# Optimization experiments

Hardware: AMD Instinct MI355X
Metric: run time of the kernel (lower is better)

Reference implementation:

```python
import jax, jax.numpy as jnp
import numpy as np

N = 50000   # total residue nodes across the batch of peptides
E = 800000  # total directed intra-peptide edges (avg degree 16)
D = 512


def _w(k, shape):
    fan_in = shape[0]
    return (jax.random.normal(k, shape, jnp.float32) / np.sqrt(fan_in)).astype(jnp.float32)


def setup_inputs() -> dict:
    key = jax.random.key(0)
    ks = jax.random.split(key, 12)
    return {
        "peptide_feature": jax.random.normal(ks[0], (N, D), jnp.float32),
        "edge_index": jax.random.randint(ks[1], (2, E), 0, N),
        # aanet_proj: 512 -> 1024 -> 1024 -> 512 -> 80 (ReLU between, none after last)
        "W1": _w(ks[2], (512, 1024)), "b1": jnp.zeros((1024,), jnp.float32),
        "W2": _w(ks[3], (1024, 1024)), "b2": jnp.zeros((1024,), jnp.float32),
        "W3": _w(ks[4], (1024, 512)), "b3": jnp.zeros((512,), jnp.float32),
        "W4": _w(ks[5], (512, 80)), "b4": jnp.zeros((80,), jnp.float32),
        # in_net: 80 -> 512
        "Win": _w(ks[6], (80, 512)), "bin_": jnp.zeros((512,), jnp.float32),
        # GIN conv MLP: 512 -> 512 -> 512 (eps = 0)
        "Wg1": _w(ks[7], (512, 512)), "bg1": jnp.zeros((512,), jnp.float32),
        "Wg2": _w(ks[8], (512, 512)), "bg2": jnp.zeros((512,), jnp.float32),
        # out_net: 512 -> 80
        "Wout": _w(ks[9], (512, 80)), "bout": jnp.zeros((80,), jnp.float32),
    }


def reference(peptide_feature, edge_index, W1, b1, W2, b2, W3, b3, W4, b4,
              Win, bin_, Wg1, bg1, Wg2, bg2, Wout, bout):
    relu = jax.nn.relu
    # aanet_proj
    h = relu(peptide_feature @ W1 + b1)
    h = relu(h @ W2 + b2)
    h = relu(h @ W3 + b3)
    peptide_feat = h @ W4 + b4                      # [N, 80]
    # in_net
    x = peptide_feat @ Win + bin_                   # [N, 512]
    # GIN message passing (sum aggregation, eps=0): per-sample loop in the
    # original is equivalent to one global pass since edges are sample-local.
    src, dst = edge_index[0], edge_index[1]
    agg = jax.ops.segment_sum(x[src], dst, num_segments=N)   # [N, 512]
    g = x + agg
    g = relu(g @ Wg1 + bg1) @ Wg2 + bg2             # GIN MLP
    # out_net
    peptide_mask = g @ Wout + bout                  # [N, 80]
    return peptide_mask, peptide_feat
```

## Files before the change

### kernel.cpp

```cpp
#include <hip/hip_runtime.h>
#include <stdint.h>


using bf16x8 = __attribute__((ext_vector_type(8))) short;
using f32x4  = __attribute__((ext_vector_type(4))) float;

__device__ inline unsigned short f2bf(float f) {
    union { float f; unsigned u; } v; v.f = f;
    unsigned u = v.u;
    u += 0x7FFFu + ((u >> 16) & 1u);
    return (unsigned short)(u >> 16);
}
__device__ inline float bf2f(unsigned u16) {
    return __uint_as_float(u16 << 16);
}

struct PreDescs {
    const float* W[8]; unsigned short* Wt[8];
    int K[8], M[8], Kp[8], ntx[8], start[8];
    int tEnd, cEnd, eEnd;
    const float* feat; unsigned short* featb; int nFeat;
    const int* ei; int E; int* cnt;
};

__global__ __launch_bounds__(256) void rg_preprocess(PreDescs d) {
    int b = blockIdx.x;
    int tid = threadIdx.x;
    if (b < d.tEnd) {
        __shared__ float t[32][33];
        int di = 0;
#pragma unroll
        for (int i = 1; i < 8; ++i) if (b >= d.start[i]) di = i;
        int local = b - d.start[di];
        int bx = local % d.ntx[di];
        int by = local / d.ntx[di];
        const float* W = d.W[di];
        unsigned short* Wt = d.Wt[di];
        int K = d.K[di], M = d.M[di], Kp = d.Kp[di];
        int mb = bx * 32, kb = by * 32;
        int tx = tid & 31, tg = tid >> 5;
#pragma unroll
        for (int p = 0; p < 4; ++p) {
            int r = tg + p * 8;
            int k = kb + r, m = mb + tx;
            t[r][tx] = (k < K && m < M) ? W[(size_t)k * M + m] : 0.f;
        }
        __syncthreads();
#pragma unroll
        for (int p = 0; p < 4; ++p) {
            int r = tg + p * 8;
            int mo = mb + r, ko = kb + tx;
            Wt[(size_t)mo * Kp + ko] = f2bf(t[tx][r]);
        }
    } else if (b < d.cEnd) {
        int i = ((b - d.tEnd) * 256 + tid) * 4;
        if (i + 3 < d.nFeat) {
            float4 v = *(const float4*)(d.feat + i);
            ushort4 o; o.x = f2bf(v.x); o.y = f2bf(v.y); o.z = f2bf(v.z); o.w = f2bf(v.w);
            *(ushort4*)(d.featb + i) = o;
        }
    } else {
        int e = (b - d.cEnd) * 256 + tid;
        if (e < d.E) atomicAdd(&d.cnt[d.ei[d.E + e]], 1);
    }
}

template <bool RELU, bool OUT_BF, bool OUT_F32, bool DEGB, int MT>
__device__ __forceinline__ void gemm_body(
    int bid,
    const unsigned short* __restrict__ A, const unsigned short* __restrict__ Bt,
    const float* __restrict__ bias, const int* __restrict__ deg, int Mvalid,
    unsigned short* __restrict__ outB, float* __restrict__ outF,
    int Nrows, int Kp, int Mp, int gN)
{
    __shared__ __align__(16) unsigned short As[128 * 64];
    __shared__ __align__(16) unsigned short Bs[128 * 64];

    int xcd = bid & 7;
    int slot = bid >> 3;
    int c = slot % MT;
    int rsub = slot / MT;
    int rt = rsub * 8 + xcd;
    if (rt >= gN) return;
    const int rowBase = rt * 128;
    const int nBase   = c * 128;

    const int tid  = threadIdx.x;
    const int lane = tid & 63;
    const int w    = tid >> 6;
    const int wm   = w & 1, wn = w >> 1;

    f32x4 acc[4][4];
#pragma unroll
    for (int i = 0; i < 4; ++i)
#pragma unroll
        for (int j = 0; j < 4; ++j) acc[i][j] = (f32x4){0.f, 0.f, 0.f, 0.f};

    const int nkt = Kp >> 6;
    for (int kt = 0; kt < nkt; ++kt) {
        __syncthreads();
        const int k0 = kt * 64;
#pragma unroll
        for (int i = 0; i < 4; ++i) {
            int q   = i * 256 + tid;
            int r   = q >> 3;
            int cbg = (q & 7) ^ (r & 7);
            const unsigned short* gp = A + (size_t)(rowBase + r) * Kp + k0 + cbg * 8;
            __builtin_amdgcn_global_load_lds(
                (const __attribute__((address_space(1))) void*)gp,
                (__attribute__((address_space(3))) void*)(&As[q * 8]), 16, 0, 0);
        }
#pragma unroll
        for (int i = 0; i < 4; ++i) {
            int q   = i * 256 + tid;
            int r   = q >> 3;
            int cbg = (q & 7) ^ (r & 7);
            const unsigned short* gp = Bt + (size_t)(nBase + r) * Kp + k0 + cbg * 8;
            __builtin_amdgcn_global_load_lds(
                (const __attribute__((address_space(1))) void*)gp,
                (__attribute__((address_space(3))) void*)(&Bs[q * 8]), 16, 0, 0);
        }
        __syncthreads();
#pragma unroll
        for (int kk = 0; kk < 2; ++kk) {
            bf16x8 a[4], b[4];
            const int cb = kk * 4 + (lane >> 4);
#pragma unroll
            for (int i = 0; i < 4; ++i) {
                int r = wm * 64 + i * 16 + (lane & 15);
                a[i] = *(const bf16x8*)&As[(r * 8 + (cb ^ (r & 7))) * 8];
            }
#pragma unroll
            for (int j = 0; j < 4; ++j) {
                int r = wn * 64 + j * 16 + (lane & 15);
                b[j] = *(const bf16x8*)&Bs[(r * 8 + (cb ^ (r & 7))) * 8];
            }
#pragma unroll
            for (int i = 0; i < 4; ++i)
#pragma unroll
                for (int j = 0; j < 4; ++j)
                    acc[i][j] = __builtin_amdgcn_mfma_f32_16x16x32_bf16(b[j], a[i], acc[i][j], 0, 0, 0);
        }
    }

    const int quad = lane >> 4;
#pragma unroll
    for (int i = 0; i < 4; ++i) {
        int row = rowBase + wm * 64 + i * 16 + (lane & 15);
        if (row >= Nrows) continue;
        float sc = 1.f;
        if (DEGB) sc = 1.f + (float)deg[row];
#pragma unroll
        for (int j = 0; j < 4; ++j) {
            int colb = nBase + wn * 64 + j * 16 + quad * 4;
            float4 bv = (colb < Mvalid) ? *(const float4*)(bias + colb)
                                        : (float4){0.f, 0.f, 0.f, 0.f};
            float v0 = acc[i][j][0] + sc * bv.x;
            float v1 = acc[i][j][1] + sc * bv.y;
            float v2 = acc[i][j][2] + sc * bv.z;
            float v3 = acc[i][j][3] + sc * bv.w;
            if (RELU) {
                v0 = v0 > 0.f ? v0 : 0.f; v1 = v1 > 0.f ? v1 : 0.f;
                v2 = v2 > 0.f ? v2 : 0.f; v3 = v3 > 0.f ? v3 : 0.f;
            }
            if (OUT_BF) {
                ushort4 o; o.x = f2bf(v0); o.y = f2bf(v1); o.z = f2bf(v2); o.w = f2bf(v3);
                *(ushort4*)(outB + (size_t)row * Mp + colb) = o;
            }
            if (OUT_F32) {
                if (colb < Mvalid)
                    *(float4*)(outF + (size_t)row * Mvalid + colb) = (float4){v0, v1, v2, v3};
            }
        }
    }
}

template <bool RELU, bool OUT_BF, bool OUT_F32, bool DEGB, int MT>
__global__ __launch_bounds__(256) void rg_gemm(
    const unsigned short* __restrict__ A, const unsigned short* __restrict__ Bt,
    const float* __restrict__ bias, const int* __restrict__ deg, int Mvalid,
    unsigned short* __restrict__ outB, float* __restrict__ outF,
    int Nrows, int Kp, int Mp, int gN)
{
    gemm_body<RELU, OUT_BF, OUT_F32, DEGB, MT>(blockIdx.x, A, Bt, bias, deg,
                                               Mvalid, outB, outF, Nrows, Kp, Mp, gN);
}

__global__ __launch_bounds__(256) void rg_gemm_l1_scatter(
    const unsigned short* __restrict__ A, const unsigned short* __restrict__ Bt,
    const float* __restrict__ bias, int Mvalid,
    unsigned short* __restrict__ outB, int Nrows, int Kp, int Mp, int gN,
    int gemmBlocks, const int* __restrict__ ei, int E,
    int* __restrict__ cursor, int* __restrict__ cols)
{
    int bid = blockIdx.x;
    if (bid < gemmBlocks) {
        gemm_body<true, true, false, false, 8>(bid, A, Bt, bias, nullptr,
                                               Mvalid, outB, nullptr, Nrows, Kp, Mp, gN);
    } else {
        int e = (bid - gemmBlocks) * 256 + threadIdx.x;
        if (e < E) {
            int d = ei[E + e];
            int p = atomicAdd(&cursor[d], 1);
            cols[p] = ei[e];
        }
    }
}

__device__ __forceinline__ void rg_gridbar(int* bar, int nb, int phase) {
    __syncthreads();
    if (threadIdx.x == 0) {
        __threadfence();
        atomicAdd(bar, 1);
        int target = phase * nb;
        while (__hip_atomic_load(bar, __ATOMIC_RELAXED, __HIP_MEMORY_SCOPE_AGENT) < target) {}
        __threadfence();
    }
    __syncthreads();
}

__global__ __launch_bounds__(1024) void rg_scan_all(
    const int* __restrict__ cnt, int* __restrict__ rowptr, int* __restrict__ cursor,
    int* __restrict__ bsums, int* bar, int Nn, int E, int nb)
{
    __shared__ int sd[1024];
    const int tid = threadIdx.x;
    const int bid = blockIdx.x;
    const int i   = bid * 1024 + tid;

    int v = (i < Nn) ? cnt[i] : 0;
    sd[tid] = v;
    __syncthreads();
    for (int off = 1; off < 1024; off <<= 1) {
        int t = (tid >= off) ? sd[tid - off] : 0;
        __syncthreads();
        sd[tid] += t;
        __syncthreads();
    }
    if (tid == 1023) bsums[bid] = sd[1023];
    rg_gridbar(bar, nb, 1);

    if (bid == 0 && tid < 64) {
        int bv = (tid < nb) ? bsums[tid] : 0;
        int incl = bv;
#pragma unroll
        for (int off = 1; off < 64; off <<= 1) {
            int t = __shfl_up(incl, off, 64);
            if (tid >= off) incl += t;
        }
        if (tid < nb) bsums[tid] = incl - bv;
    }
    rg_gridbar(bar, nb, 2);

    if (i < Nn) {
        int ex = sd[tid] - v + bsums[bid];
        rowptr[i] = ex; cursor[i] = ex;
    }
    if (i == 0) rowptr[Nn] = E;
}

__global__ __launch_bounds__(256) void rg_agg80(
    const unsigned short* __restrict__ pf, const int* __restrict__ rowptr,
    const int* __restrict__ cols, unsigned short* __restrict__ s, int Nn)
{
    int node = blockIdx.x * 4 + (threadIdx.x >> 6);
    if (node >= Nn) return;
    int lane = threadIdx.x & 63;
    const unsigned* xp = (const unsigned*)pf;
    size_t off = (size_t)node * 64 + lane;
    unsigned u = xp[off];
    float a0 = bf2f(u & 0xffffu), a1 = bf2f(u >> 16);
    int beg = rowptr[node], end = rowptr[node + 1];
    int e = beg;
    for (; e + 8 <= end; e += 8) {
        unsigned v[8];
#pragma unroll
        for (int t = 0; t < 8; ++t) v[t] = xp[(size_t)cols[e + t] * 64 + lane];
#pragma unroll
        for (int t = 0; t < 8; ++t) { a0 += bf2f(v[t] & 0xffffu); a1 += bf2f(v[t] >> 16); }
    }
    for (; e < end; ++e) {
        unsigned v = xp[(size_t)cols[e] * 64 + lane];
        a0 += bf2f(v & 0xffffu); a1 += bf2f(v >> 16);
    }
    unsigned o = (unsigned)f2bf(a0) | ((unsigned)f2bf(a1) << 16);
    ((unsigned*)s)[off] = o;
}

extern "C" void kernel_launch(void* const* d_in, const int* in_sizes, int n_in,
                              void* d_out, int out_size, void* d_ws, size_t ws_size,
                              hipStream_t stream)
{
    const float* feat = (const float*)d_in[0];
    const int*   ei   = (const int*)d_in[1];
    const float* W1 = (const float*)d_in[2];  const float* b1 = (const float*)d_in[3];
    const float* W2 = (const float*)d_in[4];  const float* b2 = (const float*)d_in[5];
    const float* W3 = (const float*)d_in[6];  const float* b3 = (const float*)d_in[7];
    const float* W4 = (const float*)d_in[8];  const float* b4 = (const float*)d_in[9];
    const float* Wi = (const float*)d_in[10]; const float* bi = (const float*)d_in[11];
    const float* Wg1 = (const float*)d_in[12]; const float* bg1 = (const float*)d_in[13];
    const float* Wg2 = (const float*)d_in[14]; const float* bg2 = (const float*)d_in[15];
    const float* Wo = (const float*)d_in[16]; const float* bo = (const float*)d_in[17];

    const int N = in_sizes[0] / 512;
    const int E = in_sizes[1] / 2;
    const int gN = (N + 127) / 128;
    const int Npad = gN * 128;

    char* ws = (char*)d_ws;
    size_t o = 0;
    auto alloc = [&](size_t bytes) { char* p = ws + o; o += (bytes + 255) & ~(size_t)255; return p; };
    unsigned short* bufA = (unsigned short*)alloc((size_t)Npad * 1024 * 2);
    unsigned short* bufB = (unsigned short*)alloc((size_t)Npad * 1024 * 2);
    unsigned short* bufC = (unsigned short*)alloc((size_t)Npad * 512 * 2);
    unsigned short* W1t = (unsigned short*)alloc((size_t)1024 * 512 * 2);
    unsigned short* W2t = (unsigned short*)alloc((size_t)1024 * 1024 * 2);
    unsigned short* W3t = (unsigned short*)alloc((size_t)512 * 1024 * 2);
    unsigned short* W4t = (unsigned short*)alloc((size_t)128 * 512 * 2);
    unsigned short* Wit = (unsigned short*)alloc((size_t)512 * 128 * 2);
    unsigned short* Wg1t = (unsigned short*)alloc((size_t)512 * 512 * 2);
    unsigned short* Wg2t = (unsigned short*)alloc((size_t)512 * 512 * 2);
    unsigned short* Wot = (unsigned short*)alloc((size_t)128 * 512 * 2);
    int* cnt    = (int*)alloc((size_t)(N + 64) * 4);
    int* bar    = cnt + N;
    int* rowptr = (int*)alloc((size_t)(N + 1) * 4);
    int* cursor = (int*)alloc((size_t)N * 4);
    int* cols   = (int*)alloc((size_t)E * 4);
    int* bsums  = (int*)alloc(256);

    float* out_mask = (float*)d_out;
    float* out_feat = (float*)d_out + (size_t)N * 80;

    hipMemsetAsync(cnt, 0, (size_t)(N + 64) * 4, stream);
    {
        PreDescs d;
        const float* Ws[8]  = {W1, W2, W3, W4, Wi, Wg1, Wg2, Wo};
        unsigned short* Ts[8] = {W1t, W2t, W3t, W4t, Wit, Wg1t, Wg2t, Wot};
        int Ks[8]  = {512, 1024, 1024, 512, 80, 512, 512, 512};
        int Ms[8]  = {1024, 1024, 512, 80, 512, 512, 512, 80};
        int Kps[8] = {512, 1024, 1024, 512, 128, 512, 512, 512};
        int Mps[8] = {1024, 1024, 512, 128, 512, 512, 512, 128};
        int st = 0;
        for (int i = 0; i < 8; ++i) {
            d.W[i] = Ws[i]; d.Wt[i] = Ts[i];
            d.K[i] = Ks[i]; d.M[i] = Ms[i]; d.Kp[i] = Kps[i];
            d.ntx[i] = Mps[i] / 32;
            d.start[i] = st;
            st += (Mps[i] / 32) * (Kps[i] / 32);
        }
        d.tEnd = st;
        d.cEnd = st + (N * 512) / 1024;
        d.eEnd = d.cEnd + (E + 255) / 256;
        d.feat = feat; d.featb = bufC; d.nFeat = N * 512;
        d.ei = ei; d.E = E; d.cnt = cnt;
        rg_preprocess<<<d.eEnd, 256, 0, stream>>>(d);
    }

    const int nb = (N + 1023) / 1024;
    rg_scan_all<<<nb, 1024, 0, stream>>>(cnt, rowptr, cursor, bsums, bar, N, E, nb);

    const int rg8 = ((gN + 7) / 8) * 8;
    auto grid = [&](int MT) { return dim3(rg8 * MT); };

    {
        const int gemmBlocks = rg8 * 8;
        const int scatBlocks = (E + 255) / 256;
        rg_gemm_l1_scatter<<<dim3(gemmBlocks + scatBlocks), 256, 0, stream>>>(
            bufC, W1t, b1, 1024, bufA, N, 512, 1024, gN,
            gemmBlocks, ei, E, cursor, cols);
    }

    rg_gemm<true, true, false, false, 8><<<grid(8), 256, 0, stream>>>(bufA, W2t, b2, nullptr, 1024, bufB, nullptr, N, 1024, 1024, gN);
    rg_gemm<true, true, false, false, 4><<<grid(4), 256, 0, stream>>>(bufB, W3t, b3, nullptr, 512, bufC, nullptr, N, 1024, 512, gN);
    rg_gemm<false, true, true, false, 1><<<grid(1), 256, 0, stream>>>(bufC, W4t, b4, nullptr, 80, bufA, out_feat, N, 512, 128, gN);

    rg_agg80<<<(N + 3) / 4, 256, 0, stream>>>(bufA, rowptr, cols, bufC, N);

    rg_gemm<false, true, false, true, 4><<<grid(4), 256, 0, stream>>>(bufC, Wit, bi, cnt, 512, bufA, nullptr, N, 128, 512, gN);
    rg_gemm<true, true, false, false, 4><<<grid(4), 256, 0, stream>>>(bufA, Wg1t, bg1, nullptr, 512, bufB, nullptr, N, 512, 512, gN);
    rg_gemm<false, true, false, false, 4><<<grid(4), 256, 0, stream>>>(bufB, Wg2t, bg2, nullptr, 512, bufC, nullptr, N, 512, 512, gN);
    rg_gemm<false, false, true, false, 1><<<grid(1), 256, 0, stream>>>(bufC, Wot, bo, nullptr, 80, nullptr, out_mask, N, 512, 128, gN);
}
```

Before: 805.2 us.

## Double-buffer GEMM LDS tiles with prefetch two k-tiles ahead

Converts the GEMM mainloop from single-buffered LDS staging to a two-stage ping-pong pipeline. The tile for step kt+2 is loaded into the buffer just consumed, with a manual vmcnt wait so global-to-LDS loads overlap MFMA compute. It also raises wave priority around the MFMA block. LDS use doubles to 64KB per block, which may reduce occupancy, and the hand-written waitcnt counts must match the number of loads issued per stage.

```diff
diff --git a/kernel.cpp b/kernel.cpp
--- a/kernel.cpp
+++ b/kernel.cpp
@@ -73,8 +73,8 @@
     unsigned short* __restrict__ outB, float* __restrict__ outF,
     int Nrows, int Kp, int Mp, int gN)
 {
-    __shared__ __align__(16) unsigned short As[128 * 64];
-    __shared__ __align__(16) unsigned short Bs[128 * 64];
+    __shared__ __align__(16) unsigned short As[2][128 * 64];
+    __shared__ __align__(16) unsigned short Bs[2][128 * 64];
 
     int xcd = bid & 7;
     int slot = bid >> 3;
@@ -97,9 +97,9 @@
         for (int j = 0; j < 4; ++j) acc[i][j] = (f32x4){0.f, 0.f, 0.f, 0.f};
 
     const int nkt = Kp >> 6;
-    for (int kt = 0; kt < nkt; ++kt) {
-        __syncthreads();
-        const int k0 = kt * 64;
+
+    auto stage = [&](int buf, int kt) {
+        const int k0 = kt << 6;
 #pragma unroll
         for (int i = 0; i < 4; ++i) {
             int q   = i * 256 + tid;
@@ -108,7 +108,7 @@
             const unsigned short* gp = A + (size_t)(rowBase + r) * Kp + k0 + cbg * 8;
             __builtin_amdgcn_global_load_lds(
                 (const __attribute__((address_space(1))) void*)gp,
-                (__attribute__((address_space(3))) void*)(&As[q * 8]), 16, 0, 0);
+                (__attribute__((address_space(3))) void*)(&As[buf][q * 8]), 16, 0, 0);
         }
 #pragma unroll
         for (int i = 0; i < 4; ++i) {
@@ -118,9 +118,19 @@
             const unsigned short* gp = Bt + (size_t)(nBase + r) * Kp + k0 + cbg * 8;
             __builtin_amdgcn_global_load_lds(
                 (const __attribute__((address_space(1))) void*)gp,
-                (__attribute__((address_space(3))) void*)(&Bs[q * 8]), 16, 0, 0);
-        }
-        __syncthreads();
+                (__attribute__((address_space(3))) void*)(&Bs[buf][q * 8]), 16, 0, 0);
+        }
+    };
+
+    stage(0, 0);
+    stage(1, 1);
+    asm volatile("s_waitcnt vmcnt(8)" ::: "memory");
+    __builtin_amdgcn_sched_barrier(0);
+    __builtin_amdgcn_s_barrier();
+    __builtin_amdgcn_sched_barrier(0);
+
+    for (int kt = 0; kt < nkt; ++kt) {
+        const int cur = kt & 1;
 #pragma unroll
         for (int kk = 0; kk < 2; ++kk) {
             bf16x8 a[4], b[4];
@@ -128,19 +138,33 @@
 #pragma unroll
             for (int i = 0; i < 4; ++i) {
                 int r = wm * 64 + i * 16 + (lane & 15);
-                a[i] = *(const bf16x8*)&As[(r * 8 + (cb ^ (r & 7))) * 8];
+                a[i] = *(const bf16x8*)&As[cur][(r * 8 + (cb ^ (r & 7))) * 8];
             }
 #pragma unroll
             for (int j = 0; j < 4; ++j) {
                 int r = wn * 64 + j * 16 + (lane & 15);
-                b[j] = *(const bf16x8*)&Bs[(r * 8 + (cb ^ (r & 7))) * 8];
+                b[j] = *(const bf16x8*)&Bs[cur][(r * 8 + (cb ^ (r & 7))) * 8];
             }
+            __builtin_amdgcn_s_setprio(1);
 #pragma unroll
             for (int i = 0; i < 4; ++i)
 #pragma unroll
                 for (int j = 0; j < 4; ++j)
                     acc[i][j] = __builtin_amdgcn_mfma_f32_16x16x32_bf16(b[j], a[i], acc[i][j], 0, 0, 0);
-        }
+            __builtin_amdgcn_s_setprio(0);
+        }
+        if (kt + 1 == nkt) break;
+        __builtin_amdgcn_sched_barrier(0);
+        __builtin_amdgcn_s_barrier();
+        if (kt + 2 < nkt) {
+            stage(cur, kt + 2);
+            asm volatile("s_waitcnt vmcnt(8)" ::: "memory");
+        } else {
+            asm volatile("s_waitcnt vmcnt(0)" ::: "memory");
+        }
+        __builtin_amdgcn_sched_barrier(0);
+        __builtin_amdgcn_s_barrier();
+        __builtin_amdgcn_sched_barrier(0);
     }
 
     const int quad = lane >> 4;
```

Result: slower. 863.6 us (+7.3%).

## Add 256x256-tile 8-wave GEMM with direct-to-LDS loads for large layers

Applied to the files above, without the earlier changes.

Introduces a new GEMM kernel using 256x256 output tiles, 512 threads, swizzled LDS double buffering fed by global_load_lds, and phased MFMA with barrier and priority control. It replaces the older 128-row GEMMs for the W1, W2, W3, Wg1 and Wg2 layers, and the fused L1+edge-scatter launch now uses 512 threads. The aim is higher arithmetic intensity and better overlap of loads with MFMA. In exchange it uses more LDS and registers per block, launches fewer blocks, and adds padding waste on the last row tile.

```diff
diff --git a/kernel.cpp b/kernel.cpp
--- a/kernel.cpp
+++ b/kernel.cpp
@@ -186,19 +186,178 @@
                                                Mvalid, outB, outF, Nrows, Kp, Mp, gN);
 }
 
-__global__ __launch_bounds__(256) void rg_gemm_l1_scatter(
+template <bool RELU, int MT>
+__device__ __forceinline__ void gemm256_body(
+    int bid,
     const unsigned short* __restrict__ A, const unsigned short* __restrict__ Bt,
-    const float* __restrict__ bias, int Mvalid,
-    unsigned short* __restrict__ outB, int Nrows, int Kp, int Mp, int gN,
+    const float* __restrict__ bias, unsigned short* __restrict__ outB,
+    int Nrows, int NrowsPad, int Kp, int Mp, int gN2)
+{
+    __shared__ __align__(16) unsigned short As[2][2][128 * 64];
+    __shared__ __align__(16) unsigned short Bs[2][2][128 * 64];
+
+    int xcd = bid & 7;
+    int slotb = bid >> 3;
+    int c = slotb % MT;
+    int rsub = slotb / MT;
+    int rt = rsub * 8 + xcd;
+    if (rt >= gN2) return;
+    const int rowBase = rt * 256;
+    const int nBase   = c * 256;
+
+    const int tid  = threadIdx.x;
+    const int lane = tid & 63;
+    const int w    = tid >> 6;
+    const int wm   = w & 1;
+    const int wn   = w >> 1;
+
+    f32x4 acc[8][4];
+#pragma unroll
+    for (int i = 0; i < 8; ++i)
+#pragma unroll
+        for (int j = 0; j < 4; ++j) acc[i][j] = (f32x4){0.f, 0.f, 0.f, 0.f};
+
+    const int nkt = Kp >> 6;
+
+    auto stageA = [&](int t, int hf) {
+        const int k0 = t << 6;
+        unsigned short* dst = &As[t & 1][hf][0];
+#pragma unroll
+        for (int ld = 0; ld < 2; ++ld) {
+            int q   = ld * 512 + tid;
+            int r   = q >> 3;
+            int cbg = (q & 7) ^ (r & 7);
+            int grow = rowBase + hf * 128 + r;
+            grow = grow < NrowsPad ? grow : NrowsPad - 1;
+            const unsigned short* gp = A + (size_t)grow * Kp + k0 + cbg * 8;
+            __builtin_amdgcn_global_load_lds(
+                (const __attribute__((address_space(1))) void*)gp,
+                (__attribute__((address_space(3))) void*)(dst + q * 8), 16, 0, 0);
+        }
+    };
+    auto stageB = [&](int t, int hf) {
+        const int k0 = t << 6;
+        unsigned short* dst = &Bs[t & 1][hf][0];
+#pragma unroll
+        for (int ld = 0; ld < 2; ++ld) {
+            int q   = ld * 512 + tid;
+            int r   = q >> 3;
+            int cbg = (q & 7) ^ (r & 7);
+            const unsigned short* gp = Bt + (size_t)(nBase + hf * 128 + r) * Kp + k0 + cbg * 8;
+            __builtin_amdgcn_global_load_lds(
+                (const __attribute__((address_space(1))) void*)gp,
+                (__attribute__((address_space(3))) void*)(dst + q * 8), 16, 0, 0);
+        }
+    };
+
+    auto phase = [&](int a, int q, int mh, int nh) {
+        const int slot = a & 1;
+        bf16x8 av[4][2], bv[2][2];
+#pragma unroll
+        for (int i = 0; i < 4; ++i) {
+            int lr = wm * 64 + i * 16 + (lane & 15);
+#pragma unroll
+            for (int kk = 0; kk < 2; ++kk) {
+                int cb = kk * 4 + (lane >> 4);
+                av[i][kk] = *(const bf16x8*)&As[slot][mh][(lr * 8 + (cb ^ (lr & 7))) * 8];
+            }
+        }
+#pragma unroll
+        for (int j = 0; j < 2; ++j) {
+            int lr = wn * 32 + j * 16 + (lane & 15);
+#pragma unroll
+            for (int kk = 0; kk < 2; ++kk) {
+                int cb = kk * 4 + (lane >> 4);
+                bv[j][kk] = *(const bf16x8*)&Bs[slot][nh][(lr * 8 + (cb ^ (lr & 7))) * 8];
+            }
+        }
+        if (q == 0) { if (a + 1 < nkt) stageA(a + 1, 1); }
+        if (q == 1) { if (a + 1 < nkt) stageB(a + 1, 1); }
+        if (q == 2) { if (a + 2 < nkt) stageA(a + 2, 0); }
+        if (q == 3) {
+            if (a + 2 < nkt) {
+                stageB(a + 2, 0);
+                asm volatile("s_waitcnt vmcnt(4)" ::: "memory");
+            } else if (a + 1 < nkt) {
+                asm volatile("s_waitcnt vmcnt(0)" ::: "memory");
+            }
+        }
+        __builtin_amdgcn_sched_barrier(0);
+        __builtin_amdgcn_s_barrier();
+        asm volatile("s_waitcnt lgkmcnt(0)" ::: "memory");
+        __builtin_amdgcn_sched_barrier(0);
+        __builtin_amdgcn_s_setprio(1);
+#pragma unroll
+        for (int i = 0; i < 4; ++i)
+#pragma unroll
+            for (int j = 0; j < 2; ++j)
+#pragma unroll
+                for (int kk = 0; kk < 2; ++kk)
+                    acc[mh * 4 + i][nh * 2 + j] = __builtin_amdgcn_mfma_f32_16x16x32_bf16(
+                        bv[j][kk], av[i][kk], acc[mh * 4 + i][nh * 2 + j], 0, 0, 0);
+        __builtin_amdgcn_s_setprio(0);
+        __builtin_amdgcn_sched_barrier(0);
+        __builtin_amdgcn_s_barrier();
+    };
+
+    stageA(0, 0); stageB(0, 0); stageA(0, 1); stageB(0, 1);
+    stageA(1, 0); stageB(1, 0);
+    asm volatile("s_waitcnt vmcnt(4)" ::: "memory");
+    __builtin_amdgcn_sched_barrier(0);
+    __builtin_amdgcn_s_barrier();
+    __builtin_amdgcn_sched_barrier(0);
+
+    for (int a = 0; a < nkt; ++a) {
+        phase(a, 0, 0, 0);
+        phase(a, 1, 0, 1);
+        phase(a, 2, 1, 0);
+        phase(a, 3, 1, 1);
+    }
+
+    const int quad = lane >> 4;
+#pragma unroll
+    for (int mi = 0; mi < 8; ++mi) {
+        int row = rowBase + ((mi >> 2) * 2 + wm) * 64 + (mi & 3) * 16 + (lane & 15);
+        if (row >= Nrows) continue;
+#pragma unroll
+        for (int nj = 0; nj < 4; ++nj) {
+            int colb = nBase + (nj >> 1) * 128 + wn * 32 + (nj & 1) * 16 + quad * 4;
+            float4 bvv = *(const float4*)(bias + colb);
+            float v0 = acc[mi][nj][0] + bvv.x;
+            float v1 = acc[mi][nj][1] + bvv.y;
+            float v2 = acc[mi][nj][2] + bvv.z;
+            float v3 = acc[mi][nj][3] + bvv.w;
+            if (RELU) {
+                v0 = v0 > 0.f ? v0 : 0.f; v1 = v1 > 0.f ? v1 : 0.f;
+                v2 = v2 > 0.f ? v2 : 0.f; v3 = v3 > 0.f ? v3 : 0.f;
+            }
+            ushort4 o; o.x = f2bf(v0); o.y = f2bf(v1); o.z = f2bf(v2); o.w = f2bf(v3);
+            *(ushort4*)(outB + (size_t)row * Mp + colb) = o;
+        }
+    }
+}
+
+template <bool RELU, int MT>
+__global__ __launch_bounds__(512) void rg_gemm256(
+    const unsigned short* __restrict__ A, const unsigned short* __restrict__ Bt,
+    const float* __restrict__ bias, unsigned short* __restrict__ outB,
+    int Nrows, int NrowsPad, int Kp, int Mp, int gN2)
+{
+    gemm256_body<RELU, MT>(blockIdx.x, A, Bt, bias, outB, Nrows, NrowsPad, Kp, Mp, gN2);
+}
+
+__global__ __launch_bounds__(512) void rg_gemm256_l1_scatter(
+    const unsigned short* __restrict__ A, const unsigned short* __restrict__ Bt,
+    const float* __restrict__ bias, unsigned short* __restrict__ outB,
+    int Nrows, int NrowsPad, int Kp, int Mp, int gN2,
     int gemmBlocks, const int* __restrict__ ei, int E,
     int* __restrict__ cursor, int* __restrict__ cols)
 {
     int bid = blockIdx.x;
     if (bid < gemmBlocks) {
-        gemm_body<true, true, false, false, 8>(bid, A, Bt, bias, nullptr,
-                                               Mvalid, outB, nullptr, Nrows, Kp, Mp, gN);
+        gemm256_body<true, 4>(bid, A, Bt, bias, outB, Nrows, NrowsPad, Kp, Mp, gN2);
     } else {
-        int e = (bid - gemmBlocks) * 256 + threadIdx.x;
+        int e = (bid - gemmBlocks) * 512 + threadIdx.x;
         if (e < E) {
             int d = ei[E + e];
             int p = atomicAdd(&cursor[d], 1);
@@ -361,23 +520,25 @@
 
     const int rg8 = ((gN + 7) / 8) * 8;
     auto grid = [&](int MT) { return dim3(rg8 * MT); };
+    const int gN2 = (N + 255) / 256;
+    const int rg256 = ((gN2 + 7) / 8) * 8;
 
     {
-        const int gemmBlocks = rg8 * 8;
-        const int scatBlocks = (E + 255) / 256;
-        rg_gemm_l1_scatter<<<dim3(gemmBlocks + scatBlocks), 256, 0, stream>>>(
-            bufC, W1t, b1, 1024, bufA, N, 512, 1024, gN,
+        const int gemmBlocks = rg256 * 4;
+        const int scatBlocks = (E + 511) / 512;
+        rg_gemm256_l1_scatter<<<dim3(gemmBlocks + scatBlocks), 512, 0, stream>>>(
+            bufC, W1t, b1, bufA, N, Npad, 512, 1024, gN2,
             gemmBlocks, ei, E, cursor, cols);
     }
 
-    rg_gemm<true, true, false, false, 8><<<grid(8), 256, 0, stream>>>(bufA, W2t, b2, nullptr, 1024, bufB, nullptr, N, 1024, 1024, gN);
-    rg_gemm<true, true, false, false, 4><<<grid(4), 256, 0, stream>>>(bufB, W3t, b3, nullptr, 512, bufC, nullptr, N, 1024, 512, gN);
+    rg_gemm256<true, 4><<<dim3(rg256 * 4), 512, 0, stream>>>(bufA, W2t, b2, bufB, N, Npad, 1024, 1024, gN2);
+    rg_gemm256<true, 2><<<dim3(rg256 * 2), 512, 0, stream>>>(bufB, W3t, b3, bufC, N, Npad, 1024, 512, gN2);
     rg_gemm<false, true, true, false, 1><<<grid(1), 256, 0, stream>>>(bufC, W4t, b4, nullptr, 80, bufA, out_feat, N, 512, 128, gN);
 
     rg_agg80<<<(N + 3) / 4, 256, 0, stream>>>(bufA, rowptr, cols, bufC, N);
 
     rg_gemm<false, true, false, true, 4><<<grid(4), 256, 0, stream>>>(bufC, Wit, bi, cnt, 512, bufA, nullptr, N, 128, 512, gN);
-    rg_gemm<true, true, false, false, 4><<<grid(4), 256, 0, stream>>>(bufA, Wg1t, bg1, nullptr, 512, bufB, nullptr, N, 512, 512, gN);
-    rg_gemm<false, true, false, false, 4><<<grid(4), 256, 0, stream>>>(bufB, Wg2t, bg2, nullptr, 512, bufC, nullptr, N, 512, 512, gN);
+    rg_gemm256<true, 2><<<dim3(rg256 * 2), 512, 0, stream>>>(bufA, Wg1t, bg1, bufB, N, Npad, 512, 512, gN2);
+    rg_gemm256<false, 2><<<dim3(rg256 * 2), 512, 0, stream>>>(bufB, Wg2t, bg2, bufC, N, Npad, 512, 512, gN2);
     rg_gemm<false, false, true, false, 1><<<grid(1), 256, 0, stream>>>(bufC, Wot, bo, nullptr, 80, nullptr, out_mask, N, 512, 128, gN);
 }
```

After: 847.5 us. 1.05x slower.
